# Kernel optimization log

Measured on AMD Instinct MI355X. Metric: run time of the kernel, lower is better.

## Reference

```python
import jax, jax.numpy as jnp
import numpy as np

SRC_V, TRG_V = 36616, 23262
EMB, ENC_H, DEC_H = 300, 512, 1024
S, T, B = 50, 50, 128


def setup_inputs() -> dict:
    key = jax.random.key(0)
    ks = jax.random.split(key, 17)
    sc = 0.05
    n = lambda k, shp: (jax.random.normal(k, shp, jnp.float32) * sc)
    return {
        "input_src_batch": jax.random.randint(ks[0], (S, B), 0, SRC_V),
        "input_trg_batch": jax.random.randint(ks[1], (T, B), 0, TRG_V),
        "EEMB": n(ks[2], (SRC_V, EMB)),
        "enc_Wih_f": n(ks[3], (4 * ENC_H, EMB)),
        "enc_Whh_f": n(ks[4], (4 * ENC_H, ENC_H)),
        "enc_b_f": n(ks[5], (4 * ENC_H,)),
        "enc_Wih_r": n(ks[6], (4 * ENC_H, EMB)),
        "enc_Whh_r": n(ks[7], (4 * ENC_H, ENC_H)),
        "enc_b_r": n(ks[8], (4 * ENC_H,)),
        "attn_Wi": n(ks[9], (DEC_H, DEC_H)),
        "attn_Wo": n(ks[10], (DEC_H, 2 * DEC_H)),
        "dec_Wih": n(ks[11], (4 * DEC_H, DEC_H + EMB)),
        "dec_Whh": n(ks[12], (4 * DEC_H, DEC_H)),
        "dec_b": n(ks[13], (4 * DEC_H,)),
        "DEMB": n(ks[14], (TRG_V, EMB)),
        "gen_W": n(ks[15], (TRG_V, DEC_H)),
        "gen_b": n(ks[16], (TRG_V,)),
    }


def lstm_step(h, c, x, Wih, Whh, b):
    # PyTorch gate order: i, f, g, o
    g = x @ Wih.T + h @ Whh.T + b
    i, f, gg, o = jnp.split(g, 4, axis=-1)
    c2 = jax.nn.sigmoid(f) * c + jax.nn.sigmoid(i) * jnp.tanh(gg)
    h2 = jax.nn.sigmoid(o) * jnp.tanh(c2)
    return h2, c2


def reference(input_src_batch, input_trg_batch, EEMB, enc_Wih_f, enc_Whh_f,
              enc_b_f, enc_Wih_r, enc_Whh_r, enc_b_r, attn_Wi, attn_Wo,
              dec_Wih, dec_Whh, dec_b, DEMB, gen_W, gen_b):
    batch = input_src_batch.shape[1]
    sent_len = input_trg_batch.shape[0]
    emb = EEMB[input_src_batch]  # [S, B, 300]

    def scan_dir(xs, Wih, Whh, b):
        def f(carry, x):
            h, c = carry
            h2, c2 = lstm_step(h, c, x, Wih, Whh, b)
            return (h2, c2), h2
        init = (jnp.zeros((batch, ENC_H), emb.dtype),
                jnp.zeros((batch, ENC_H), emb.dtype))
        (hF, cF), hs = jax.lax.scan(f, init, xs)
        return hs, hF, cF

    hs_f, hF, cF = scan_dir(emb, enc_Wih_f, enc_Whh_f, enc_b_f)
    hs_r, hR, cR = scan_dir(emb[::-1], enc_Wih_r, enc_Whh_r, enc_b_r)
    hs_r = hs_r[::-1]
    enc_out = jnp.concatenate([hs_f, hs_r], axis=-1)  # [S, B, 1024]
    # torch permute(1,2,0).view(B,1024) interleaves fwd/rev per feature
    hidden = jnp.stack([hF, hR], axis=-1).reshape(batch, DEC_H)
    context = jnp.stack([cF, cR], axis=-1).reshape(batch, DEC_H)

    def attn(h):
        semi = h @ attn_Wi.T                                # [B,1024]
        score = jnp.einsum('sbd,bd->sb', enc_out, semi)     # [S,B]
        alpha = jax.nn.softmax(score, axis=0)               # softmax over src len
        s_tilde = jnp.einsum('sb,sbd->bd', alpha, enc_out)  # [B,1024]
        return jnp.tanh(jnp.concatenate([s_tilde, h], axis=1) @ attn_Wo.T)

    trg_emb = DEMB[input_trg_batch[: sent_len - 1]]  # [T-1, B, 300]

    def step(carry, x_emb):
        h, c = carry
        c_t = attn(h)
        dec_in = jnp.concatenate([c_t, x_emb], axis=1)  # [B, 1324]
        h2, c2 = lstm_step(h, c, dec_in, dec_Wih, dec_Whh, dec_b)
        logp = jax.nn.log_softmax(h2 @ gen_W.T + gen_b, axis=1)
        return (h2, c2), logp

    _, outs = jax.lax.scan(step, (hidden, context), trg_emb)  # [T-1,B,V]
    out0 = jnp.zeros((1, batch, TRG_V), outs.dtype)
    return jnp.concatenate([out0, outs], axis=0)  # [T, B, V]
```

## Files before the change

kernel.cpp:

```cpp
#include <hip/hip_runtime.h>
#include <hip/hip_bf16.h>
#include <hip/hip_fp16.h>

#define S_LEN 50
#define T_LEN 50
#define BATCH 128
#define EMB 300
#define ENC_H 512
#define DEC_H 1024
#define TRG_V 23262
#define DEC_IN (DEC_H + EMB)
#define KCAT (DEC_IN + DEC_H)
#define GN (4 * DEC_H)

static inline int cdiv(int a, int b) { return (a + b - 1) / b; }

__device__ __forceinline__ float sigm(float x) { return 1.f / (1.f + expf(-x)); }
__device__ __forceinline__ float b2f(unsigned short u) {
    union { float f; unsigned u; } c; c.u = ((unsigned)u) << 16; return c.f;
}
__device__ __forceinline__ float h2f(unsigned short u) {
    __half_raw r; r.x = u; return __half2float(*(const __half*)&r);
}

typedef __attribute__((ext_vector_type(8))) short bf16x8;
typedef __attribute__((ext_vector_type(4))) float f32x4;

__device__ __forceinline__ void gload_lds16(const void* g, void* l) {
    __builtin_amdgcn_global_load_lds((const __attribute__((address_space(1))) int*)g,
                                     (__attribute__((address_space(3))) int*)l, 16, 0, 0);
}

__device__ __forceinline__ float cload1(const float* p) {
    return __hip_atomic_load(p, __ATOMIC_RELAXED, __HIP_MEMORY_SCOPE_AGENT);
}
__device__ __forceinline__ float2 cload2(const float* p) {
    unsigned long long u = __hip_atomic_load((const unsigned long long*)p,
                                             __ATOMIC_RELAXED, __HIP_MEMORY_SCOPE_AGENT);
    union U { unsigned long long u; float2 f; } c; c.u = u; return c.f;
}
__device__ __forceinline__ float4 cload4(const float* p) {
    float2 a = cload2(p), b = cload2(p + 2);
    return make_float4(a.x, a.y, b.x, b.y);
}
__device__ __forceinline__ void cstore1(float* p, float v) {
    __hip_atomic_store(p, v, __ATOMIC_RELAXED, __HIP_MEMORY_SCOPE_AGENT);
}
__device__ __forceinline__ void cstore2(float* p, float2 v) {
    union U { unsigned long long u; float2 f; } c; c.f = v;
    __hip_atomic_store((unsigned long long*)p, c.u, __ATOMIC_RELAXED, __HIP_MEMORY_SCOPE_AGENT);
}
__device__ __forceinline__ void cstore4(float* p, float4 v) {
    cstore2(p, make_float2(v.x, v.y)); cstore2(p + 2, make_float2(v.z, v.w));
}

__device__ __forceinline__ void gbar(unsigned* cnt, unsigned target) {
    __syncthreads();
    if (threadIdx.x == 0) {
        atomicAdd(cnt, 1u);
        while (atomicAdd(cnt, 0u) < target)
            __builtin_amdgcn_s_sleep(32);
    }
    __syncthreads();
}

__global__ __launch_bounds__(256)
void gemm_mfma_bf16(const __hip_bfloat16* __restrict__ A, const __hip_bfloat16* __restrict__ W,
                    const float* __restrict__ bias, float* __restrict__ C,
                    int M, int N, int K, int ldc)
{
    __shared__ short As[128 * 32];
    __shared__ short Bs[128 * 32];
    const int tid  = threadIdx.x;
    const int wave = tid >> 6;
    const int lane = tid & 63;
    const int m0 = blockIdx.y * 128;
    const int n0 = blockIdx.x * 128;
    const int wr = wave >> 1, wc = wave & 1;

    const int srow = lane >> 2;
    const int kgrp = lane & 3;
    const int arow0 = 32 * wave;

    f32x4 acc[4][4] = {};

    for (int k0 = 0; k0 < K; k0 += 32) {
#pragma unroll
        for (int c = 0; c < 2; c++) {
            int row = arow0 + 16 * c + srow;
            gload_lds16(A + (size_t)(m0 + row) * K + k0 + kgrp * 8,
                        &As[(arow0 + 16 * c) * 32]);
        }
#pragma unroll
        for (int c = 0; c < 2; c++) {
            int row = arow0 + 16 * c + srow;
            int gr = n0 + row; if (gr > N - 1) gr = N - 1;
            gload_lds16(W + (size_t)gr * K + k0 + kgrp * 8,
                        &Bs[(arow0 + 16 * c) * 32]);
        }
        __syncthreads();

        bf16x8 a[4], b[4];
#pragma unroll
        for (int mi = 0; mi < 4; mi++)
            a[mi] = *(const bf16x8*)&As[(wr * 64 + mi * 16 + (lane & 15)) * 32 + (lane >> 4) * 8];
#pragma unroll
        for (int ni = 0; ni < 4; ni++)
            b[ni] = *(const bf16x8*)&Bs[(wc * 64 + ni * 16 + (lane & 15)) * 32 + (lane >> 4) * 8];
#pragma unroll
        for (int mi = 0; mi < 4; mi++)
#pragma unroll
            for (int ni = 0; ni < 4; ni++)
                acc[mi][ni] = __builtin_amdgcn_mfma_f32_16x16x32_bf16(a[mi], b[ni], acc[mi][ni], 0, 0, 0);
        __syncthreads();
    }

#pragma unroll
    for (int mi = 0; mi < 4; mi++)
#pragma unroll
        for (int ni = 0; ni < 4; ni++) {
            int col = n0 + wc * 64 + ni * 16 + (lane & 15);
            if (col >= N) continue;
            float bv = bias[col];
#pragma unroll
            for (int r = 0; r < 4; r++) {
                int row = m0 + wr * 64 + mi * 16 + (lane >> 4) * 4 + r;
                C[(size_t)row * ldc + col] = acc[mi][ni][r] + bv;
            }
        }
}

__global__ void cast_f32_bf16(const float* __restrict__ in, __hip_bfloat16* __restrict__ out, size_t n)
{
    size_t i = ((size_t)blockIdx.x * blockDim.x + threadIdx.x) * 4;
    if (i + 3 < n) {
        float4 v = *(const float4*)(in + i);
        out[i + 0] = __float2bfloat16(v.x);
        out[i + 1] = __float2bfloat16(v.y);
        out[i + 2] = __float2bfloat16(v.z);
        out[i + 3] = __float2bfloat16(v.w);
    } else {
        for (; i < n; i++) out[i] = __float2bfloat16(in[i]);
    }
}

__global__ void cast_f32_fp16(const float* __restrict__ in, __half* __restrict__ out, size_t n)
{
    size_t i = ((size_t)blockIdx.x * blockDim.x + threadIdx.x) * 4;
    if (i + 3 < n) {
        float4 v = *(const float4*)(in + i);
        out[i + 0] = __float2half(v.x);
        out[i + 1] = __float2half(v.y);
        out[i + 2] = __float2half(v.z);
        out[i + 3] = __float2half(v.w);
    } else {
        for (; i < n; i++) out[i] = __float2half(in[i]);
    }
}

template<int BM, int BN, int BK, int TM, int TN, bool HAS_BIAS>
__global__ __launch_bounds__((BM / TM) * (BN / TN))
void gemm_bt(const float* __restrict__ A, const float* __restrict__ W, int ldw,
             const float* __restrict__ bias, float* __restrict__ C,
             int M, int N, int K, int ldc)
{
    constexpr int NT  = (BM / TM) * (BN / TN);
    constexpr int NGA = TM / 4;
    constexpr int NGB = TN / 4;
    constexpr int GS  = (BN / TN) * 4;
    constexpr int LPA = BM * BK / 4 / NT;
    constexpr int LPB = BN * BK / 4 / NT;

    __shared__ float As[BK][BM + 4];
    __shared__ float Bs[BK][BN + 4];

    const int tid = threadIdx.x;
    const int tx = tid % (BN / TN);
    const int ty = tid / (BN / TN);
    const int m0 = blockIdx.y * BM;
    const int n0 = blockIdx.x * BN;

    float acc[TM][TN];
#pragma unroll
    for (int i = 0; i < TM; i++)
#pragma unroll
        for (int j = 0; j < TN; j++) acc[i][j] = 0.f;

    for (int k0 = 0; k0 < K; k0 += BK) {
#pragma unroll
        for (int e = 0; e < LPA; e++) {
            int idx = tid + e * NT;
            int r = idx / (BK / 4);
            int c4 = idx % (BK / 4);
            int row = m0 + r; if (row > M - 1) row = M - 1;
            int kk = k0 + c4 * 4;
            float4 v;
            if (kk + 3 < K) {
                v = *(const float4*)(A + (size_t)row * K + kk);
            } else {
                v.x = (kk + 0 < K) ? A[(size_t)row * K + kk + 0] : 0.f;
                v.y = (kk + 1 < K) ? A[(size_t)row * K + kk + 1] : 0.f;
                v.z = (kk + 2 < K) ? A[(size_t)row * K + kk + 2] : 0.f;
                v.w = (kk + 3 < K) ? A[(size_t)row * K + kk + 3] : 0.f;
            }
            As[c4 * 4 + 0][r] = v.x; As[c4 * 4 + 1][r] = v.y;
            As[c4 * 4 + 2][r] = v.z; As[c4 * 4 + 3][r] = v.w;
        }
#pragma unroll
        for (int e = 0; e < LPB; e++) {
            int idx = tid + e * NT;
            int r = idx / (BK / 4);
            int c4 = idx % (BK / 4);
            int row = n0 + r; if (row > N - 1) row = N - 1;
            int kk = k0 + c4 * 4;
            float4 v;
            if (kk + 3 < K) {
                v = *(const float4*)(W + (size_t)row * ldw + kk);
            } else {
                v.x = (kk + 0 < K) ? W[(size_t)row * ldw + kk + 0] : 0.f;
                v.y = (kk + 1 < K) ? W[(size_t)row * ldw + kk + 1] : 0.f;
                v.z = (kk + 2 < K) ? W[(size_t)row * ldw + kk + 2] : 0.f;
                v.w = (kk + 3 < K) ? W[(size_t)row * ldw + kk + 3] : 0.f;
            }
            Bs[c4 * 4 + 0][r] = v.x; Bs[c4 * 4 + 1][r] = v.y;
            Bs[c4 * 4 + 2][r] = v.z; Bs[c4 * 4 + 3][r] = v.w;
        }
        __syncthreads();
#pragma unroll
        for (int kk = 0; kk < BK; kk++) {
            float a[TM], b[TN];
#pragma unroll
            for (int g = 0; g < NGA; g++) {
                float4 v = *(const float4*)(&As[kk][ty * TM + g * 4]);
                a[g * 4 + 0] = v.x; a[g * 4 + 1] = v.y; a[g * 4 + 2] = v.z; a[g * 4 + 3] = v.w;
            }
#pragma unroll
            for (int g = 0; g < NGB; g++) {
                float4 v = *(const float4*)(&Bs[kk][tx * 4 + g * GS]);
                b[g * 4 + 0] = v.x; b[g * 4 + 1] = v.y; b[g * 4 + 2] = v.z; b[g * 4 + 3] = v.w;
            }
#pragma unroll
            for (int i = 0; i < TM; i++)
#pragma unroll
                for (int j = 0; j < TN; j++)
                    acc[i][j] = fmaf(a[i], b[j], acc[i][j]);
        }
        __syncthreads();
    }

#pragma unroll
    for (int i = 0; i < TM; i++) {
        int row = m0 + ty * TM + i;
        if (row >= M) continue;
#pragma unroll
        for (int g = 0; g < NGB; g++) {
            int colb = n0 + tx * 4 + g * GS;
#pragma unroll
            for (int j = 0; j < 4; j++) {
                int cc = colb + j;
                if (cc >= N) continue;
                float v = acc[i][g * 4 + j];
                if (HAS_BIAS) v += bias[cc];
                C[(size_t)row * ldc + cc] = v;
            }
        }
    }
}

__device__ __forceinline__ float4 load4B(const float* p) { return *(const float4*)p; }
__device__ __forceinline__ float4 load4B(const __half* p) {
    ushort4 v = *(const ushort4*)p;
    return make_float4(h2f(v.x), h2f(v.y), h2f(v.z), h2f(v.w));
}
__device__ __forceinline__ float ld1B(const float* p) { return *p; }
__device__ __forceinline__ float ld1B(const __half* p) { return h2f(*(const unsigned short*)p); }

template<typename TB>
__device__ __forceinline__ float4 g4kB(const TB* base, int kk, int K) {
    float4 v = make_float4(0.f, 0.f, 0.f, 0.f);
    if (kk + 3 < K) v = load4B(base + kk);
    else {
        if (kk     < K) v.x = ld1B(base + kk);
        if (kk + 1 < K) v.y = ld1B(base + kk + 1);
        if (kk + 2 < K) v.z = ld1B(base + kk + 2);
    }
    return v;
}
__device__ __forceinline__ float4 g4kc(const float* base, int kk, int K) {
    float4 v = make_float4(0.f, 0.f, 0.f, 0.f);
    if (kk + 3 < K) v = cload4(base + kk);
    else {
        if (kk     < K) v.x = cload1(base + kk);
        if (kk + 1 < K) v.y = cload1(base + kk + 1);
        if (kk + 2 < K) v.z = cload1(base + kk + 2);
    }
    return v;
}

template<typename TB>
__device__ __forceinline__ void tile_core(
    float (&As)[2][32][36], float (&Bs)[2][32][68],
    const float* __restrict__ A, int lda,
    const TB* __restrict__ W, int ldw, int K,
    int m0, int n0, float (&acc)[2][4])
{
    const int tid = threadIdx.x;
    const int tx = tid & 15, ty = tid >> 4;
    const int ar = tid >> 3, ac4 = tid & 7;
    const float* abase = A + (size_t)(m0 + ar) * lda;
    const TB* bb0      = W + (size_t)(n0 + ar) * ldw;
    const TB* bb1      = bb0 + (size_t)32 * ldw;

    acc[0][0]=acc[0][1]=acc[0][2]=acc[0][3]=0.f;
    acc[1][0]=acc[1][1]=acc[1][2]=acc[1][3]=0.f;
    const int NIT = (K + 31) / 32;

    float4 pa, pb0, pb1;
    {
        int kk = ac4 * 4;
        pa  = cload4(abase + kk);
        pb0 = load4B(bb0 + kk);
        pb1 = load4B(bb1 + kk);
    }
    *(float4*)&As[0][ar][ac4 * 4] = pa;
    Bs[0][ac4*4+0][ar]    = pb0.x; Bs[0][ac4*4+1][ar]    = pb0.y;
    Bs[0][ac4*4+2][ar]    = pb0.z; Bs[0][ac4*4+3][ar]    = pb0.w;
    Bs[0][ac4*4+0][ar+32] = pb1.x; Bs[0][ac4*4+1][ar+32] = pb1.y;
    Bs[0][ac4*4+2][ar+32] = pb1.z; Bs[0][ac4*4+3][ar+32] = pb1.w;
    __syncthreads();

    int cur = 0;
    for (int it = 0; it < NIT; ++it) {
        float4 qa, qb0, qb1;
        const bool has = (it + 1 < NIT);
        if (has) {
            int k0 = (it + 1) * 32;
            int kk = k0 + ac4 * 4;
            if (k0 + 32 <= K) { qa = cload4(abase + kk); qb0 = load4B(bb0 + kk); qb1 = load4B(bb1 + kk); }
            else { qa = g4kc(abase, kk, K); qb0 = g4kB(bb0, kk, K); qb1 = g4kB(bb1, kk, K); }
        }
#pragma unroll
        for (int k4 = 0; k4 < 8; ++k4) {
            float4 a0 = *(const float4*)&As[cur][ty*2+0][k4*4];
            float4 a1 = *(const float4*)&As[cur][ty*2+1][k4*4];
            float4 b0 = *(const float4*)&Bs[cur][k4*4+0][tx*4];
            float4 b1 = *(const float4*)&Bs[cur][k4*4+1][tx*4];
            float4 b2 = *(const float4*)&Bs[cur][k4*4+2][tx*4];
            float4 b3 = *(const float4*)&Bs[cur][k4*4+3][tx*4];
            float av0[4] = {a0.x, a0.y, a0.z, a0.w};
            float av1[4] = {a1.x, a1.y, a1.z, a1.w};
            float4 bq[4] = {b0, b1, b2, b3};
#pragma unroll
            for (int q = 0; q < 4; q++) {
                acc[0][0] = fmaf(av0[q], bq[q].x, acc[0][0]);
                acc[0][1] = fmaf(av0[q], bq[q].y, acc[0][1]);
                acc[0][2] = fmaf(av0[q], bq[q].z, acc[0][2]);
                acc[0][3] = fmaf(av0[q], bq[q].w, acc[0][3]);
                acc[1][0] = fmaf(av1[q], bq[q].x, acc[1][0]);
                acc[1][1] = fmaf(av1[q], bq[q].y, acc[1][1]);
                acc[1][2] = fmaf(av1[q], bq[q].z, acc[1][2]);
                acc[1][3] = fmaf(av1[q], bq[q].w, acc[1][3]);
            }
        }
        if (has) {
            int nb = cur ^ 1;
            *(float4*)&As[nb][ar][ac4 * 4] = qa;
            Bs[nb][ac4*4+0][ar]    = qb0.x; Bs[nb][ac4*4+1][ar]    = qb0.y;
            Bs[nb][ac4*4+2][ar]    = qb0.z; Bs[nb][ac4*4+3][ar]    = qb0.w;
            Bs[nb][ac4*4+0][ar+32] = qb1.x; Bs[nb][ac4*4+1][ar+32] = qb1.y;
            Bs[nb][ac4*4+2][ar+32] = qb1.z; Bs[nb][ac4*4+3][ar+32] = qb1.w;
        }
        __syncthreads();
        cur ^= 1;
    }
}

__device__ __forceinline__ void attn_body(
    int b, float* hv, float* sc,
    const __half* __restrict__ encP, const __half* __restrict__ enc_out,
    float* __restrict__ attn_cat)
{
    const int tid = threadIdx.x;
    for (int d = tid; d < DEC_H; d += 256) hv[d] = cload1(&attn_cat[(size_t)b * 2 * DEC_H + DEC_H + d]);
    __syncthreads();
    int wave = tid >> 6, lane = tid & 63;
    for (int s = wave; s < S_LEN; s += 4) {
        const unsigned short* e = (const unsigned short*)(encP + ((size_t)s * BATCH + b) * DEC_H);
        float p = 0.f;
        for (int d = lane; d < DEC_H; d += 64) p = fmaf(h2f(e[d]), hv[d], p);
        for (int off = 32; off; off >>= 1) p += __shfl_down(p, off);
        if (lane == 0) sc[s] = p;
    }
    __syncthreads();
    if (tid < 64) {
        float x = (tid < S_LEN) ? sc[tid] : -1e30f;
        float m = x;
        for (int off = 32; off; off >>= 1) m = fmaxf(m, __shfl_xor(m, off));
        float ex = (tid < S_LEN) ? expf(x - m) : 0.f;
        float ssum = ex;
        for (int off = 32; off; off >>= 1) ssum += __shfl_xor(ssum, off);
        if (tid < S_LEN) sc[tid] = ex / ssum;
    }
    __syncthreads();
    for (int d = tid; d < DEC_H; d += 256) {
        float a = 0.f;
        const unsigned short* eo = (const unsigned short*)enc_out;
#pragma unroll 5
        for (int s = 0; s < S_LEN; s++)
            a = fmaf(sc[s], h2f(eo[((size_t)s * BATCH + b) * DEC_H + d]), a);
        cstore1(&attn_cat[(size_t)b * 2 * DEC_H + d], a);
    }
}

__global__ __launch_bounds__(256)
void enc_persistent(const float* __restrict__ Gf, const float* __restrict__ Gr,
                    const float* __restrict__ whhF, const float* __restrict__ whhR,
                    float* __restrict__ hF2, float* __restrict__ hR2,
                    float* __restrict__ cF, float* __restrict__ cR,
                    float* __restrict__ enc_out, unsigned* __restrict__ barcnt)
{
    __shared__ struct { float As[2][32][36]; float Bs[2][32][68]; } sm;
    const int blk = blockIdx.x;
    const int tid = threadIdx.x;
    const int tx = tid & 15, ty = tid >> 4;
    const int dir = blk >> 7;
    const int id  = blk & 127;
    const int m0 = (id >> 5) * 32;
    const int n0 = (id & 31) * 64;
    const float* W  = dir ? whhR : whhF;
    float* cst      = dir ? cR : cF;
    float* hbase    = dir ? hR2 : hF2;
    const float* G  = dir ? Gr : Gf;
    const int HS = BATCH * ENC_H;
    unsigned epoch = 0;
    float acc[2][4];

    for (int t = 0; t < S_LEN; ++t) {
        const float* h_in = hbase + (size_t)(t & 1) * HS;
        float* h_out      = hbase + (size_t)((t + 1) & 1) * HS;
        int s_g = dir ? (S_LEN - 1 - t) : t;
        const float* D = G + (size_t)s_g * BATCH * 4 * ENC_H;

        tile_core<float>(sm.As, sm.Bs, h_in, ENC_H, W, ENC_H, ENC_H, m0, n0, acc);

        int cb = n0 + tx * 4, j = cb >> 2;
#pragma unroll
        for (int i = 0; i < 2; i++) {
            int b = m0 + ty * 2 + i;
            float4 d4 = *(const float4*)(D + (size_t)b * 4 * ENC_H + cb);
            float gi = acc[i][0] + d4.x, gf = acc[i][1] + d4.y;
            float gg = acc[i][2] + d4.z, go = acc[i][3] + d4.w;
            float c2 = sigm(gf) * cst[b * ENC_H + j] + sigm(gi) * tanhf(gg);
            float h2 = sigm(go) * tanhf(c2);
            cst[b * ENC_H + j] = c2;
            cstore1(&h_out[b * ENC_H + j], h2);
            enc_out[((size_t)s_g * BATCH + b) * DEC_H + dir * ENC_H + j] = h2;
        }
        if (t < S_LEN - 1) gbar(barcnt, 256u * (++epoch));
    }
}

__global__ __launch_bounds__(256)
void dec_persistent(const __half* __restrict__ encP, const __half* __restrict__ enc_out,
                    const int* __restrict__ trg, const float* __restrict__ DEMB,
                    const __half* __restrict__ aWo, const __half* __restrict__ wcat,
                    const float* __restrict__ db_i,
                    float* __restrict__ attn_cat, float* __restrict__ catA,
                    float* __restrict__ cdec, float* __restrict__ gpart,
                    __hip_bfloat16* __restrict__ H_bf, unsigned* __restrict__ barcnt)
{
    __shared__ union {
        struct { float hv[DEC_H]; float sc[S_LEN]; } a;
        struct { float As[2][32][36]; float Bs[2][32][68]; } g;
    } sm;
    const int blk = blockIdx.x;
    const int tid = threadIdx.x;
    const int tx = tid & 15, ty = tid >> 4;
    unsigned epoch = 0;
    float acc[2][4];

    for (int t = 0; t < T_LEN - 1; ++t) {
        if (blk < 128) {
            attn_body(blk, sm.a.hv, sm.a.sc, encP, enc_out, attn_cat);
        } else if (blk < 192) {
            int id = blk - 128;
            int m0 = (id >> 4) * 32, n0 = (id & 15) * 64;
            tile_core<__half>(sm.g.As, sm.g.Bs, attn_cat + DEC_H, 2 * DEC_H,
                              aWo + DEC_H, 2 * DEC_H, DEC_H, m0, n0, acc);
            int cb = n0 + tx * 4;
#pragma unroll
            for (int i = 0; i < 2; i++) {
                int row = m0 + ty * 2 + i;
                cstore4(catA + (size_t)row * KCAT + cb,
                        make_float4(acc[i][0], acc[i][1], acc[i][2], acc[i][3]));
            }
        } else {
            int tau = blk - 192;
            int m0 = (tau >> 6) * 32, n0 = (tau & 63) * 64;
            tile_core<__half>(sm.g.As, sm.g.Bs, catA + DEC_H, KCAT,
                              wcat + DEC_H, KCAT, KCAT - DEC_H, m0, n0, acc);
            int cb = n0 + tx * 4;
#pragma unroll
            for (int i = 0; i < 2; i++) {
                int row = m0 + ty * 2 + i;
                cstore4(gpart + (size_t)row * GN + cb,
                        make_float4(acc[i][0], acc[i][1], acc[i][2], acc[i][3]));
            }
        }
        gbar(barcnt, 256u * (++epoch));

        if (blk < 64) {
            int m0 = (blk >> 4) * 32, n0 = (blk & 15) * 64;
            tile_core<__half>(sm.g.As, sm.g.Bs, attn_cat, 2 * DEC_H,
                              aWo, 2 * DEC_H, DEC_H, m0, n0, acc);
            int cb = n0 + tx * 4;
#pragma unroll
            for (int i = 0; i < 2; i++) {
                int row = m0 + ty * 2 + i;
                float* dst = catA + (size_t)row * KCAT + cb;
                float4 prev = cload4(dst);
                cstore4(dst, make_float4(tanhf(acc[i][0] + prev.x), tanhf(acc[i][1] + prev.y),
                                         tanhf(acc[i][2] + prev.z), tanhf(acc[i][3] + prev.w)));
            }
        } else {
            int tau = blk;
            int m0 = (tau >> 6) * 32, n0 = (tau & 63) * 64;
            tile_core<__half>(sm.g.As, sm.g.Bs, catA + DEC_H, KCAT,
                              wcat + DEC_H, KCAT, KCAT - DEC_H, m0, n0, acc);
            int cb = n0 + tx * 4;
#pragma unroll
            for (int i = 0; i < 2; i++) {
                int row = m0 + ty * 2 + i;
                cstore4(gpart + (size_t)row * GN + cb,
                        make_float4(acc[i][0], acc[i][1], acc[i][2], acc[i][3]));
            }
        }
        gbar(barcnt, 256u * (++epoch));

        {
            int m0 = (blk >> 6) * 32, n0 = (blk & 63) * 64;
            tile_core<__half>(sm.g.As, sm.g.Bs, catA, KCAT, wcat, KCAT, DEC_H, m0, n0, acc);
            int cb = n0 + tx * 4, j = cb >> 2;
            float4 bz = *(const float4*)(db_i + cb);
#pragma unroll
            for (int i = 0; i < 2; i++) {
                int b = m0 + ty * 2 + i;
                float4 gp = cload4(gpart + (size_t)b * GN + cb);
                float gi = acc[i][0] + gp.x + bz.x, gf = acc[i][1] + gp.y + bz.y;
                float gg = acc[i][2] + gp.z + bz.z, go = acc[i][3] + gp.w + bz.w;
                float c2 = sigm(gf) * cdec[b * DEC_H + j] + sigm(gi) * tanhf(gg);
                float h2 = sigm(go) * tanhf(c2);
                cdec[b * DEC_H + j] = c2;
                H_bf[(size_t)t * BATCH * DEC_H + b * DEC_H + j] = __float2bfloat16(h2);
                cstore1(&attn_cat[(size_t)b * 2 * DEC_H + DEC_H + j], h2);
                cstore1(&catA[(size_t)b * KCAT + DEC_IN + j], h2);
            }
            if ((blk & 63) == 0 && t + 1 < T_LEN - 1) {
                for (int idx = tid; idx < 32 * EMB; idx += 256) {
                    int r = m0 + idx / EMB, e = idx % EMB;
                    int idt = trg[(t + 1) * BATCH + r];
                    cstore1(&catA[(size_t)r * KCAT + DEC_H + e], DEMB[(size_t)idt * EMB + e]);
                }
            }
        }
        if (t < T_LEN - 2) gbar(barcnt, 256u * (++epoch));
    }
}

__global__ void zero_f32(float* p, size_t n) {
    size_t i = (size_t)blockIdx.x * blockDim.x + threadIdx.x;
    if (i < n) p[i] = 0.f;
}

__global__ void gather_rows(const int* __restrict__ ids, const float* __restrict__ E,
                            float* __restrict__ out, int nrows, int width)
{
    size_t i = (size_t)blockIdx.x * blockDim.x + threadIdx.x;
    size_t total = (size_t)nrows * width;
    if (i >= total) return;
    int r = (int)(i / width);
    int e = (int)(i % width);
    out[i] = E[(size_t)ids[r] * width + e];
}

__global__ void interleave_rows(const float* __restrict__ src, float* __restrict__ dst,
                                int units, int kdim)
{
    size_t i = (size_t)blockIdx.x * blockDim.x + threadIdx.x;
    size_t total = (size_t)4 * units * kdim;
    if (i >= total) return;
    int ir = (int)(i / kdim), k = (int)(i % kdim);
    int gate = ir & 3, j = ir >> 2;
    dst[i] = src[(size_t)(gate * units + j) * kdim + k];
}

__global__ void interleave_vec(const float* __restrict__ src, float* __restrict__ dst, int units)
{
    int i = blockIdx.x * blockDim.x + threadIdx.x;
    if (i >= 4 * units) return;
    int gate = i & 3, j = i >> 2;
    dst[i] = src[gate * units + j];
}

__global__ void build_wcat_fp16(const float* __restrict__ Wih, const float* __restrict__ Whh,
                                __half* __restrict__ dst)
{
    size_t i = (size_t)blockIdx.x * blockDim.x + threadIdx.x;
    if (i >= (size_t)GN * KCAT) return;
    int ir = (int)(i / KCAT), k = (int)(i % KCAT);
    int gate = ir & 3, j = ir >> 2;
    int r = gate * DEC_H + j;
    float v = (k < DEC_IN) ? Wih[(size_t)r * DEC_IN + k] : Whh[(size_t)r * DEC_H + (k - DEC_IN)];
    dst[i] = __float2half(v);
}

__global__ void transpose_sq(const float* __restrict__ src, float* __restrict__ dst, int n)
{
    int i = blockIdx.x * blockDim.x + threadIdx.x;
    if (i >= n * n) return;
    int r = i / n, c = i % n;
    dst[(size_t)r * n + c] = src[(size_t)c * n + r];
}

__global__ void dec_init2(const float* __restrict__ hF, const float* __restrict__ cF,
                          const float* __restrict__ hR, const float* __restrict__ cR,
                          const int* __restrict__ trg, const float* __restrict__ DEMB,
                          float* __restrict__ attn_cat, float* __restrict__ catA,
                          float* __restrict__ cdec)
{
    int idx = blockIdx.x * blockDim.x + threadIdx.x;
    if (idx < BATCH * DEC_H) {
        int b = idx / DEC_H, j = idx % DEC_H;
        int half = j >> 1;
        float h = (j & 1) ? hR[b * ENC_H + half] : hF[b * ENC_H + half];
        float c = (j & 1) ? cR[b * ENC_H + half] : cF[b * ENC_H + half];
        attn_cat[(size_t)b * 2 * DEC_H + DEC_H + j] = h;
        catA[(size_t)b * KCAT + DEC_IN + j] = h;
        cdec[idx] = c;
    } else {
        int i = idx - BATCH * DEC_H;
        if (i >= BATCH * EMB) return;
        int b = i / EMB, e = i % EMB;
        catA[(size_t)b * KCAT + DEC_H + e] = DEMB[(size_t)trg[b] * EMB + e];
    }
}

__global__ __launch_bounds__(256)
void log_softmax_rows(float* __restrict__ X, int V)
{
    int row = blockIdx.x;
    float* x = X + (size_t)row * V;
    int tid = threadIdx.x;
    __shared__ float redm[4], reds[4];
    float m = -1e30f;
    for (int i = tid; i < V; i += 256) m = fmaxf(m, x[i]);
    for (int off = 32; off; off >>= 1) m = fmaxf(m, __shfl_xor(m, off));
    if ((tid & 63) == 0) redm[tid >> 6] = m;
    __syncthreads();
    m = fmaxf(fmaxf(redm[0], redm[1]), fmaxf(redm[2], redm[3]));
    float s = 0.f;
    for (int i = tid; i < V; i += 256) s += expf(x[i] - m);
    for (int off = 32; off; off >>= 1) s += __shfl_xor(s, off);
    if ((tid & 63) == 0) reds[tid >> 6] = s;
    __syncthreads();
    s = reds[0] + reds[1] + reds[2] + reds[3];
    float lg = m + logf(s);
    for (int i = tid; i < V; i += 256) x[i] -= lg;
}

static void launch_gemm_big_bias(const float* A, const float* W, int ldw, const float* bias,
                                 float* C, int M, int N, int K, int ldc, hipStream_t s)
{
    dim3 g(cdiv(N, 128), cdiv(M, 128), 1);
    gemm_bt<128, 128, 16, 8, 8, true><<<g, 256, 0, s>>>(A, W, ldw, bias, C, M, N, K, ldc);
}
static void launch_gemm_big(const float* A, const float* W, int ldw, float* C,
                            int M, int N, int K, int ldc, hipStream_t s)
{
    dim3 g(cdiv(N, 128), cdiv(M, 128), 1);
    gemm_bt<128, 128, 16, 8, 8, false><<<g, 256, 0, s>>>(A, W, ldw, nullptr, C, M, N, K, ldc);
}

extern "C" void kernel_launch(void* const* d_in, const int* in_sizes, int n_in,
                              void* d_out, int out_size, void* d_ws, size_t ws_size,
                              hipStream_t stream)
{
    const int*   src   = (const int*)d_in[0];
    const int*   trg   = (const int*)d_in[1];
    const float* EEMBp = (const float*)d_in[2];
    const float* eWihF = (const float*)d_in[3];
    const float* eWhhF = (const float*)d_in[4];
    const float* ebF   = (const float*)d_in[5];
    const float* eWihR = (const float*)d_in[6];
    const float* eWhhR = (const float*)d_in[7];
    const float* ebR   = (const float*)d_in[8];
    const float* aWi   = (const float*)d_in[9];
    const float* aWo   = (const float*)d_in[10];
    const float* dWih  = (const float*)d_in[11];
    const float* dWhh  = (const float*)d_in[12];
    const float* db    = (const float*)d_in[13];
    const float* DEMBp = (const float*)d_in[14];
    const float* gW    = (const float*)d_in[15];
    const float* gb    = (const float*)d_in[16];
    float* out = (float*)d_out;
    float* ws  = (float*)d_ws;

    size_t off = 0;
    auto alloc = [&](size_t n) { float* p = ws + off; off += n; return p; };

    float* Gf      = alloc((size_t)S_LEN * BATCH * 4 * ENC_H);
    float* Gr      = alloc((size_t)S_LEN * BATCH * 4 * ENC_H);
    float* emb_src = alloc((size_t)S_LEN * BATCH * EMB);
    float* enc_out = alloc((size_t)S_LEN * BATCH * DEC_H);
    float* hF2     = alloc((size_t)2 * BATCH * ENC_H);
    float* hR2     = alloc((size_t)2 * BATCH * ENC_H);
    float* cF      = alloc(BATCH * ENC_H);
    float* cR      = alloc(BATCH * ENC_H);
    float* wihF_i  = alloc((size_t)4 * ENC_H * EMB);
    float* wihR_i  = alloc((size_t)4 * ENC_H * EMB);
    float* whhF_i  = alloc((size_t)4 * ENC_H * ENC_H);
    float* whhR_i  = alloc((size_t)4 * ENC_H * ENC_H);
    float* ebF_i   = alloc(4 * ENC_H);
    float* ebR_i   = alloc(4 * ENC_H);
    float* db_i    = alloc(4 * DEC_H);
    float* aWiT    = alloc((size_t)DEC_H * DEC_H);
    float* cdec    = alloc(BATCH * DEC_H);
    float* attn_cat= alloc((size_t)BATCH * 2 * DEC_H);
    float* catA    = alloc((size_t)BATCH * KCAT);
    float* gpart   = alloc((size_t)BATCH * GN);
    __half* wcat_hf = (__half*)alloc((size_t)GN * KCAT / 2);
    __half* aWo_hf  = (__half*)alloc((size_t)DEC_H * 2 * DEC_H / 2);
    __half* encP_hf = (__half*)alloc((size_t)S_LEN * BATCH * DEC_H / 2);
    __half* eout_hf = (__half*)alloc((size_t)S_LEN * BATCH * DEC_H / 2);
    __hip_bfloat16* H_bf = (__hip_bfloat16*)alloc((size_t)(T_LEN - 1) * BATCH * DEC_H / 2);
    unsigned* barcnt = (unsigned*)alloc(16);
    __hip_bfloat16* gWb = (__hip_bfloat16*)Gf;
    float* encP = Gr;

    const int HS = BATCH * ENC_H;

    zero_f32<<<cdiv(BATCH * TRG_V, 256), 256, 0, stream>>>(out, (size_t)BATCH * TRG_V);
    zero_f32<<<cdiv(6 * HS, 256), 256, 0, stream>>>(hF2, (size_t)6 * HS);
    zero_f32<<<1, 16, 0, stream>>>((float*)barcnt, 16);

    gather_rows<<<cdiv(S_LEN * BATCH * EMB, 256), 256, 0, stream>>>(src, EEMBp, emb_src, S_LEN * BATCH, EMB);

    interleave_rows<<<cdiv(4 * ENC_H * EMB, 256), 256, 0, stream>>>(eWihF, wihF_i, ENC_H, EMB);
    interleave_rows<<<cdiv(4 * ENC_H * EMB, 256), 256, 0, stream>>>(eWihR, wihR_i, ENC_H, EMB);
    interleave_rows<<<cdiv(4 * ENC_H * ENC_H, 256), 256, 0, stream>>>(eWhhF, whhF_i, ENC_H, ENC_H);
    interleave_rows<<<cdiv(4 * ENC_H * ENC_H, 256), 256, 0, stream>>>(eWhhR, whhR_i, ENC_H, ENC_H);
    interleave_vec<<<cdiv(4 * ENC_H, 256), 256, 0, stream>>>(ebF, ebF_i, ENC_H);
    interleave_vec<<<cdiv(4 * ENC_H, 256), 256, 0, stream>>>(ebR, ebR_i, ENC_H);
    build_wcat_fp16<<<cdiv(GN * KCAT, 256), 256, 0, stream>>>(dWih, dWhh, wcat_hf);
    cast_f32_fp16<<<cdiv((int)((size_t)DEC_H * 2 * DEC_H / 4), 256), 256, 0, stream>>>(
        aWo, aWo_hf, (size_t)DEC_H * 2 * DEC_H);
    interleave_vec<<<cdiv(4 * DEC_H, 256), 256, 0, stream>>>(db, db_i, DEC_H);
    transpose_sq<<<cdiv(DEC_H * DEC_H, 256), 256, 0, stream>>>(aWi, aWiT, DEC_H);

    launch_gemm_big_bias(emb_src, wihF_i, EMB, ebF_i, Gf, S_LEN * BATCH, 4 * ENC_H, EMB, 4 * ENC_H, stream);
    launch_gemm_big_bias(emb_src, wihR_i, EMB, ebR_i, Gr, S_LEN * BATCH, 4 * ENC_H, EMB, 4 * ENC_H, stream);

    enc_persistent<<<256, 256, 0, stream>>>(Gf, Gr, whhF_i, whhR_i, hF2, hR2, cF, cR,
                                            enc_out, &barcnt[0]);

    launch_gemm_big(enc_out, aWiT, DEC_H, encP, S_LEN * BATCH, DEC_H, DEC_H, DEC_H, stream);
    cast_f32_fp16<<<cdiv((int)((size_t)S_LEN * BATCH * DEC_H / 4), 256), 256, 0, stream>>>(
        encP, encP_hf, (size_t)S_LEN * BATCH * DEC_H);
    cast_f32_fp16<<<cdiv((int)((size_t)S_LEN * BATCH * DEC_H / 4), 256), 256, 0, stream>>>(
        enc_out, eout_hf, (size_t)S_LEN * BATCH * DEC_H);

    cast_f32_bf16<<<cdiv((int)((size_t)TRG_V * DEC_H / 4), 256), 256, 0, stream>>>(gW, gWb, (size_t)TRG_V * DEC_H);

    dec_init2<<<cdiv(BATCH * DEC_H + BATCH * EMB, 256), 256, 0, stream>>>(
        hF2, cF, hR2, cR, trg, DEMBp, attn_cat, catA, cdec);

    dec_persistent<<<256, 256, 0, stream>>>(encP_hf, eout_hf, trg, DEMBp, aWo_hf, wcat_hf, db_i,
                                            attn_cat, catA, cdec, gpart, H_bf, &barcnt[1]);

    {
        dim3 g(cdiv(TRG_V, 128), cdiv((T_LEN - 1) * BATCH, 128), 1);
        gemm_mfma_bf16<<<g, 256, 0, stream>>>(H_bf, gWb, gb, out + (size_t)BATCH * TRG_V,
                                              (T_LEN - 1) * BATCH, TRG_V, DEC_H, TRG_V);
    }

    log_softmax_rows<<<(T_LEN - 1) * BATCH, 256, 0, stream>>>(out + (size_t)BATCH * TRG_V, TRG_V);
}
```

Measured before the change: 12.59 ms.

## Double decoder persistent kernel threads and use 64-deep K tiles

```diff
diff --git a/kernel.cpp b/kernel.cpp
--- a/kernel.cpp
+++ b/kernel.cpp
@@ -297,19 +297,18 @@
     return v;
 }
 
-template<typename TB>
 __device__ __forceinline__ void tile_core(
     float (&As)[2][32][36], float (&Bs)[2][32][68],
     const float* __restrict__ A, int lda,
-    const TB* __restrict__ W, int ldw, int K,
+    const float* __restrict__ W, int ldw, int K,
     int m0, int n0, float (&acc)[2][4])
 {
     const int tid = threadIdx.x;
     const int tx = tid & 15, ty = tid >> 4;
     const int ar = tid >> 3, ac4 = tid & 7;
     const float* abase = A + (size_t)(m0 + ar) * lda;
-    const TB* bb0      = W + (size_t)(n0 + ar) * ldw;
-    const TB* bb1      = bb0 + (size_t)32 * ldw;
+    const float* bb0   = W + (size_t)(n0 + ar) * ldw;
+    const float* bb1   = bb0 + (size_t)32 * ldw;
 
     acc[0][0]=acc[0][1]=acc[0][2]=acc[0][3]=0.f;
     acc[1][0]=acc[1][1]=acc[1][2]=acc[1][3]=0.f;
@@ -375,16 +374,87 @@
     }
 }
 
+__device__ __forceinline__ void tile_core512(
+    float (&As)[2][32][68], float (&Bs)[2][64][68],
+    const float* __restrict__ A, int lda,
+    const __half* __restrict__ W, int ldw, int K,
+    int m0, int n0, float (&acc)[4])
+{
+    const int tid = threadIdx.x;
+    const int tx = tid & 15, ty = tid >> 4;
+    const int ar = tid >> 4, ac4 = tid & 15;
+    const int br = tid >> 3 & 63, bc4 = tid & 7;
+    const float* abase = A + (size_t)(m0 + ar) * lda;
+    const __half* bbase = W + (size_t)(n0 + br) * ldw;
+
+    acc[0]=acc[1]=acc[2]=acc[3]=0.f;
+    const int NIT = (K + 63) / 64;
+
+    float4 pa, pb0, pb1;
+    auto LOAD = [&](int it, float4& qa, float4& qb0, float4& qb1) {
+        int k0 = it * 64;
+        int kA = k0 + ac4 * 4;
+        int kB0 = k0 + bc4 * 4, kB1 = kB0 + 32;
+        if (k0 + 64 <= K) {
+            qa = cload4(abase + kA);
+            qb0 = load4B(bbase + kB0);
+            qb1 = load4B(bbase + kB1);
+        } else {
+            qa = g4kc(abase, kA, K);
+            qb0 = g4kB(bbase, kB0, K);
+            qb1 = g4kB(bbase, kB1, K);
+        }
+    };
+    auto SLDS = [&](int nb, const float4& qa, const float4& qb0, const float4& qb1) {
+        *(float4*)&As[nb][ar][ac4 * 4] = qa;
+        Bs[nb][bc4*4+0][br]      = qb0.x; Bs[nb][bc4*4+1][br]      = qb0.y;
+        Bs[nb][bc4*4+2][br]      = qb0.z; Bs[nb][bc4*4+3][br]      = qb0.w;
+        Bs[nb][bc4*4+32][br]     = qb1.x; Bs[nb][bc4*4+33][br]     = qb1.y;
+        Bs[nb][bc4*4+34][br]     = qb1.z; Bs[nb][bc4*4+35][br]     = qb1.w;
+    };
+
+    LOAD(0, pa, pb0, pb1);
+    SLDS(0, pa, pb0, pb1);
+    __syncthreads();
+
+    int cur = 0;
+    for (int it = 0; it < NIT; ++it) {
+        float4 qa, qb0, qb1;
+        const bool has = (it + 1 < NIT);
+        if (has) LOAD(it + 1, qa, qb0, qb1);
+#pragma unroll
+        for (int k4 = 0; k4 < 16; ++k4) {
+            float4 av = *(const float4*)&As[cur][ty][k4*4];
+            float4 b0 = *(const float4*)&Bs[cur][k4*4+0][tx*4];
+            float4 b1 = *(const float4*)&Bs[cur][k4*4+1][tx*4];
+            float4 b2 = *(const float4*)&Bs[cur][k4*4+2][tx*4];
+            float4 b3 = *(const float4*)&Bs[cur][k4*4+3][tx*4];
+            float avq[4] = {av.x, av.y, av.z, av.w};
+            float4 bq[4] = {b0, b1, b2, b3};
+#pragma unroll
+            for (int q = 0; q < 4; q++) {
+                acc[0] = fmaf(avq[q], bq[q].x, acc[0]);
+                acc[1] = fmaf(avq[q], bq[q].y, acc[1]);
+                acc[2] = fmaf(avq[q], bq[q].z, acc[2]);
+                acc[3] = fmaf(avq[q], bq[q].w, acc[3]);
+            }
+        }
+        if (has) SLDS(cur ^ 1, qa, qb0, qb1);
+        __syncthreads();
+        cur ^= 1;
+    }
+}
+
 __device__ __forceinline__ void attn_body(
     int b, float* hv, float* sc,
     const __half* __restrict__ encP, const __half* __restrict__ enc_out,
     float* __restrict__ attn_cat)
 {
     const int tid = threadIdx.x;
-    for (int d = tid; d < DEC_H; d += 256) hv[d] = cload1(&attn_cat[(size_t)b * 2 * DEC_H + DEC_H + d]);
+    for (int d = tid; d < DEC_H; d += 512) hv[d] = cload1(&attn_cat[(size_t)b * 2 * DEC_H + DEC_H + d]);
     __syncthreads();
     int wave = tid >> 6, lane = tid & 63;
-    for (int s = wave; s < S_LEN; s += 4) {
+    for (int s = wave; s < S_LEN; s += 8) {
         const unsigned short* e = (const unsigned short*)(encP + ((size_t)s * BATCH + b) * DEC_H);
         float p = 0.f;
         for (int d = lane; d < DEC_H; d += 64) p = fmaf(h2f(e[d]), hv[d], p);
@@ -402,7 +472,7 @@
         if (tid < S_LEN) sc[tid] = ex / ssum;
     }
     __syncthreads();
-    for (int d = tid; d < DEC_H; d += 256) {
+    for (int d = tid; d < DEC_H; d += 512) {
         float a = 0.f;
         const unsigned short* eo = (const unsigned short*)enc_out;
 #pragma unroll 5
@@ -441,7 +511,7 @@
         int s_g = dir ? (S_LEN - 1 - t) : t;
         const float* D = G + (size_t)s_g * BATCH * 4 * ENC_H;
 
-        tile_core<float>(sm.As, sm.Bs, h_in, ENC_H, W, ENC_H, ENC_H, m0, n0, acc);
+        tile_core(sm.As, sm.Bs, h_in, ENC_H, W, ENC_H, ENC_H, m0, n0, acc);
 
         int cb = n0 + tx * 4, j = cb >> 2;
 #pragma unroll
@@ -460,7 +530,7 @@
     }
 }
 
-__global__ __launch_bounds__(256)
+__global__ __launch_bounds__(512)
 void dec_persistent(const __half* __restrict__ encP, const __half* __restrict__ enc_out,
                     const int* __restrict__ trg, const float* __restrict__ DEMB,
                     const __half* __restrict__ aWo, const __half* __restrict__ wcat,
@@ -471,13 +541,13 @@
 {
     __shared__ union {
         struct { float hv[DEC_H]; float sc[S_LEN]; } a;
-        struct { float As[2][32][36]; float Bs[2][32][68]; } g;
+        struct { float As[2][32][68]; float Bs[2][64][68]; } g;
     } sm;
     const int blk = blockIdx.x;
     const int tid = threadIdx.x;
     const int tx = tid & 15, ty = tid >> 4;
     unsigned epoch = 0;
-    float acc[2][4];
+    float acc[4];
 
     for (int t = 0; t < T_LEN - 1; ++t) {
         if (blk < 128) {
@@ -485,78 +555,59 @@
         } else if (blk < 192) {
             int id = blk - 128;
             int m0 = (id >> 4) * 32, n0 = (id & 15) * 64;
-            tile_core<__half>(sm.g.As, sm.g.Bs, attn_cat + DEC_H, 2 * DEC_H,
-                              aWo + DEC_H, 2 * DEC_H, DEC_H, m0, n0, acc);
-            int cb = n0 + tx * 4;
-#pragma unroll
-            for (int i = 0; i < 2; i++) {
-                int row = m0 + ty * 2 + i;
-                cstore4(catA + (size_t)row * KCAT + cb,
-                        make_float4(acc[i][0], acc[i][1], acc[i][2], acc[i][3]));
-            }
+            tile_core512(sm.g.As, sm.g.Bs, attn_cat + DEC_H, 2 * DEC_H,
+                         aWo + DEC_H, 2 * DEC_H, DEC_H, m0, n0, acc);
+            int cb = n0 + tx * 4, row = m0 + ty;
+            cstore4(catA + (size_t)row * KCAT + cb,
+                    make_float4(acc[0], acc[1], acc[2], acc[3]));
         } else {
             int tau = blk - 192;
             int m0 = (tau >> 6) * 32, n0 = (tau & 63) * 64;
-            tile_core<__half>(sm.g.As, sm.g.Bs, catA + DEC_H, KCAT,
-                              wcat + DEC_H, KCAT, KCAT - DEC_H, m0, n0, acc);
-            int cb = n0 + tx * 4;
-#pragma unroll
-            for (int i = 0; i < 2; i++) {
-                int row = m0 + ty * 2 + i;
-                cstore4(gpart + (size_t)row * GN + cb,
-                        make_float4(acc[i][0], acc[i][1], acc[i][2], acc[i][3]));
-            }
+            tile_core512(sm.g.As, sm.g.Bs, catA + DEC_H, KCAT,
+                         wcat + DEC_H, KCAT, KCAT - DEC_H, m0, n0, acc);
+            int cb = n0 + tx * 4, row = m0 + ty;
+            cstore4(gpart + (size_t)row * GN + cb,
+                    make_float4(acc[0], acc[1], acc[2], acc[3]));
         }
         gbar(barcnt, 256u * (++epoch));
 
         if (blk < 64) {
             int m0 = (blk >> 4) * 32, n0 = (blk & 15) * 64;
-            tile_core<__half>(sm.g.As, sm.g.Bs, attn_cat, 2 * DEC_H,
-                              aWo, 2 * DEC_H, DEC_H, m0, n0, acc);
-            int cb = n0 + tx * 4;
-#pragma unroll
-            for (int i = 0; i < 2; i++) {
-                int row = m0 + ty * 2 + i;
-                float* dst = catA + (size_t)row * KCAT + cb;
-                float4 prev = cload4(dst);
-                cstore4(dst, make_float4(tanhf(acc[i][0] + prev.x), tanhf(acc[i][1] + prev.y),
-                                         tanhf(acc[i][2] + prev.z), tanhf(acc[i][3] + prev.w)));
-            }
+            tile_core512(sm.g.As, sm.g.Bs, attn_cat, 2 * DEC_H,
+                         aWo, 2 * DEC_H, DEC_H, m0, n0, acc);
+            int cb = n0 + tx * 4, row = m0 + ty;
+            float* dst = catA + (size_t)row * KCAT + cb;
+            float4 prev = cload4(dst);
+            cstore4(dst, make_float4(tanhf(acc[0] + prev.x), tanhf(acc[1] + prev.y),
+                                     tanhf(acc[2] + prev.z), tanhf(acc[3] + prev.w)));
         } else {
             int tau = blk;
             int m0 = (tau >> 6) * 32, n0 = (tau & 63) * 64;
-            tile_core<__half>(sm.g.As, sm.g.Bs, catA + DEC_H, KCAT,
-                              wcat + DEC_H, KCAT, KCAT - DEC_H, m0, n0, acc);
-            int cb = n0 + tx * 4;
-#pragma unroll
-            for (int i = 0; i < 2; i++) {
-                int row = m0 + ty * 2 + i;
-                cstore4(gpart + (size_t)row * GN + cb,
-                        make_float4(acc[i][0], acc[i][1], acc[i][2], acc[i][3]));
-            }
+            tile_core512(sm.g.As, sm.g.Bs, catA + DEC_H, KCAT,
+                         wcat + DEC_H, KCAT, KCAT - DEC_H, m0, n0, acc);
+            int cb = n0 + tx * 4, row = m0 + ty;
+            cstore4(gpart + (size_t)row * GN + cb,
+                    make_float4(acc[0], acc[1], acc[2], acc[3]));
         }
         gbar(barcnt, 256u * (++epoch));
 
         {
             int m0 = (blk >> 6) * 32, n0 = (blk & 63) * 64;
-            tile_core<__half>(sm.g.As, sm.g.Bs, catA, KCAT, wcat, KCAT, DEC_H, m0, n0, acc);
+            tile_core512(sm.g.As, sm.g.Bs, catA, KCAT, wcat, KCAT, DEC_H, m0, n0, acc);
             int cb = n0 + tx * 4, j = cb >> 2;
             float4 bz = *(const float4*)(db_i + cb);
-#pragma unroll
-            for (int i = 0; i < 2; i++) {
-                int b = m0 + ty * 2 + i;
-                float4 gp = cload4(gpart + (size_t)b * GN + cb);
-                float gi = acc[i][0] + gp.x + bz.x, gf = acc[i][1] + gp.y + bz.y;
-                float gg = acc[i][2] + gp.z + bz.z, go = acc[i][3] + gp.w + bz.w;
-                float c2 = sigm(gf) * cdec[b * DEC_H + j] + sigm(gi) * tanhf(gg);
-                float h2 = sigm(go) * tanhf(c2);
-                cdec[b * DEC_H + j] = c2;
-                H_bf[(size_t)t * BATCH * DEC_H + b * DEC_H + j] = __float2bfloat16(h2);
-                cstore1(&attn_cat[(size_t)b * 2 * DEC_H + DEC_H + j], h2);
-                cstore1(&catA[(size_t)b * KCAT + DEC_IN + j], h2);
-            }
+            int b = m0 + ty;
+            float4 gp = cload4(gpart + (size_t)b * GN + cb);
+            float gi = acc[0] + gp.x + bz.x, gf = acc[1] + gp.y + bz.y;
+            float gg = acc[2] + gp.z + bz.z, go = acc[3] + gp.w + bz.w;
+            float c2 = sigm(gf) * cdec[b * DEC_H + j] + sigm(gi) * tanhf(gg);
+            float h2 = sigm(go) * tanhf(c2);
+            cdec[b * DEC_H + j] = c2;
+            H_bf[(size_t)t * BATCH * DEC_H + b * DEC_H + j] = __float2bfloat16(h2);
+            cstore1(&attn_cat[(size_t)b * 2 * DEC_H + DEC_H + j], h2);
+            cstore1(&catA[(size_t)b * KCAT + DEC_IN + j], h2);
             if ((blk & 63) == 0 && t + 1 < T_LEN - 1) {
-                for (int idx = tid; idx < 32 * EMB; idx += 256) {
+                for (int idx = tid; idx < 32 * EMB; idx += 512) {
                     int r = m0 + idx / EMB, e = idx % EMB;
                     int idt = trg[(t + 1) * BATCH + r];
                     cstore1(&catA[(size_t)r * KCAT + DEC_H + e], DEMB[(size_t)idt * EMB + e]);
@@ -774,7 +825,7 @@
     dec_init2<<<cdiv(BATCH * DEC_H + BATCH * EMB, 256), 256, 0, stream>>>(
         hF2, cF, hR2, cR, trg, DEMBp, attn_cat, catA, cdec);
 
-    dec_persistent<<<256, 256, 0, stream>>>(encP_hf, eout_hf, trg, DEMBp, aWo_hf, wcat_hf, db_i,
+    dec_persistent<<<256, 512, 0, stream>>>(encP_hf, eout_hf, trg, DEMBp, aWo_hf, wcat_hf, db_i,
                                             attn_cat, catA, cdec, gpart, H_bf, &barcnt[1]);
 
     {
```

New measurement: 13.27 ms. 1.05x slower.
